# Kernel tuning notes

Hardware: AMD Instinct MI355X
Metric: run time of the kernel (lower is better)

The kernel has to match this reference:

```python
import jax, jax.numpy as jnp
import numpy as np
from jax import lax

BN_EPS = 1e-5


def _spatial_gate(x, w, g, b, m, v):
    # x: [N, C, H, W]; ChannelPool -> [N, 2, H, W]; 7x7 conv -> [N,1,H,W]; BN (eval); sigmoid gate
    comp = jnp.stack([jnp.max(x, axis=1), jnp.mean(x, axis=1)], axis=1)
    o = lax.conv_general_dilated(comp, w, (1, 1), [(3, 3), (3, 3)],
                                 dimension_numbers=('NCHW', 'OIHW', 'NCHW'))
    o = (o - m[None, :, None, None]) * lax.rsqrt(v + BN_EPS)[None, :, None, None] \
        * g[None, :, None, None] + b[None, :, None, None]
    s = jax.nn.sigmoid(o)
    return x * s


def _eca_sort(x, w_eca):
    # global avg pool -> sort channels desc -> 1D conv over sorted seq -> sigmoid -> unsort -> gate
    y = jnp.mean(x, axis=(2, 3))               # [N, C]
    order = jnp.argsort(-y, axis=1)            # descending sort indices
    rank = jnp.argsort(order, axis=1)          # inverse permutation
    ys = jnp.take_along_axis(y, order, axis=1)  # sorted descending
    k = w_eca.shape[-1]
    p = k // 2
    o = lax.conv_general_dilated(ys[:, None, :], w_eca, (1,), [(p, p)],
                                 dimension_numbers=('NCH', 'OIH', 'NCH'))[:, 0, :]
    sig = jax.nn.sigmoid(o)
    yr = jnp.take_along_axis(sig, rank, axis=1)  # reorder back per original index_select(rank)
    return x * yr[:, :, None, None]


def setup_inputs() -> dict:
    key = jax.random.key(0)
    ks = jax.random.split(key, 6)
    N, C, H, W = 32, 256, 56, 56
    inp = {
        'x': jax.random.normal(ks[0], (N, C, H, W), dtype=jnp.float32),
        'weight': jax.random.normal(ks[1], (1,), dtype=jnp.float32),
        'w_h': jax.random.normal(ks[2], (1, 2, 7, 7), dtype=jnp.float32) * 0.1,
        'g_h': jnp.ones((1,), jnp.float32), 'b_h': jnp.zeros((1,), jnp.float32),
        'm_h': jnp.zeros((1,), jnp.float32), 'v_h': jnp.ones((1,), jnp.float32),
        'w_w': jax.random.normal(ks[3], (1, 2, 7, 7), dtype=jnp.float32) * 0.1,
        'g_w': jnp.ones((1,), jnp.float32), 'b_w': jnp.zeros((1,), jnp.float32),
        'm_w': jnp.zeros((1,), jnp.float32), 'v_w': jnp.ones((1,), jnp.float32),
        'w_s': jax.random.normal(ks[4], (1, 2, 7, 7), dtype=jnp.float32) * 0.1,
        'g_s': jnp.ones((1,), jnp.float32), 'b_s': jnp.zeros((1,), jnp.float32),
        'm_s': jnp.zeros((1,), jnp.float32), 'v_s': jnp.ones((1,), jnp.float32),
        'w_eca': jax.random.normal(ks[5], (1, 1, 5), dtype=jnp.float32) * 0.3,
    }
    return inp


def reference(x, weight, w_h, g_h, b_h, m_h, v_h, w_w, g_w, b_w, m_w, v_w,
              w_s, g_s, b_s, m_s, v_s, w_eca):
    # branch 1: gate over H-as-channel (permute 0,2,1,3)
    xh = jnp.transpose(x, (0, 2, 1, 3))
    x11 = jnp.transpose(_spatial_gate(xh, w_h, g_h, b_h, m_h, v_h), (0, 2, 1, 3))
    # branch 2: gate over W-as-channel (permute 0,3,2,1)
    xw = jnp.transpose(x, (0, 3, 2, 1))
    x21 = jnp.transpose(_spatial_gate(xw, w_w, g_w, b_w, m_w, v_w), (0, 3, 2, 1))
    # branch 3: eca with sort/unsort
    x31 = _eca_sort(x, w_eca)
    # branch 4: plain spatial gate
    xo = _spatial_gate(x, w_s, g_s, b_s, m_s, v_s)
    return 0.23779 * xo + 0.24695 * x11 + 0.24365 * x21 + 0.27173 * x31
```

## Files before the change

### kernel.cpp

```cpp
#include <hip/hip_runtime.h>
#include <math.h>

#define N_ 32
#define C_ 256
#define H_ 56
#define W_ 56
#define HW_ (H_*W_)
#define HW4_ (HW_/4)
#define CHW_ (C_*HW_)
#define CHW4_ (CHW_/4)
#define NHW_ (N_*HW_)
#define NHW4_ (NHW_/4)
#define NCW_ (N_*C_*W_)
#define NHC_ (N_*H_*C_)
#define BN_EPS_ 1e-5f

#define TLD 57

#define F4MAX(a,b) do { (a).x=fmaxf((a).x,(b).x); (a).y=fmaxf((a).y,(b).y); \
                        (a).z=fmaxf((a).z,(b).z); (a).w=fmaxf((a).w,(b).w); } while(0)
#define F4ADD(a,b) do { (a).x+=(b).x; (a).y+=(b).y; (a).z+=(b).z; (a).w+=(b).w; } while(0)

__global__ __launch_bounds__(64) void plane_k(
        const float* __restrict__ x,
        float* __restrict__ maxH, float* __restrict__ meanH,
        float* __restrict__ maxWt, float* __restrict__ meanWt,
        float* __restrict__ y) {
    __shared__ float tile[H_ * TLD];
    const int wid = blockIdx.x;
    const int lane = threadIdx.x;
    const int n = wid >> 8, c = wid & 255;
    const float4* x4 = (const float4*)x + (size_t)wid * HW4_;

    float4 r[12], rl;
    #pragma unroll
    for (int i = 0; i < 12; ++i) r[i] = x4[i * 64 + lane];
    if (lane < 16) rl = x4[768 + lane];
    #pragma unroll
    for (int i = 0; i < 12; ++i) {
        int u = i * 64 + lane;
        int row = u / 14, c0 = (u - row * 14) * 4;
        float* d = &tile[row * TLD + c0];
        d[0] = r[i].x; d[1] = r[i].y; d[2] = r[i].z; d[3] = r[i].w;
    }
    if (lane < 16) {
        int u = 768 + lane;
        int row = u / 14, c0 = (u - row * 14) * 4;
        float* d = &tile[row * TLD + c0];
        d[0] = rl.x; d[1] = rl.y; d[2] = rl.z; d[3] = rl.w;
    }
    float csm = 0.f;
    if (lane < W_) {
        float cmx = -INFINITY;
        #pragma unroll 8
        for (int j = 0; j < H_; ++j) {
            float v = tile[j * TLD + lane];
            cmx = fmaxf(cmx, v); csm += v;
        }
        int o = (n * C_ + c) * W_ + lane;
        maxH[o] = cmx;
        meanH[o] = csm * (1.f / H_);
    }
    float ysum = (lane < W_) ? csm : 0.f;
    #pragma unroll
    for (int off = 32; off >= 1; off >>= 1) ysum += __shfl_xor(ysum, off);
    if (lane == 0) y[n * C_ + c] = ysum * (1.f / HW_);
    if (lane < H_) {
        const float* rp = &tile[lane * TLD];
        float rmx = -INFINITY, rsm = 0.f;
        #pragma unroll 8
        for (int j = 0; j < W_; ++j) {
            float v = rp[j];
            rmx = fmaxf(rmx, v); rsm += v;
        }
        int o = (n * C_ + c) * H_ + lane;
        maxWt[o] = rmx;
        meanWt[o] = rsm * (1.f / W_);
    }
}

__global__ __launch_bounds__(256) void cpool_k(
        const float* __restrict__ x,
        float* __restrict__ maxC, float* __restrict__ meanC) {
    __shared__ float4 smx[256];
    __shared__ float4 ssm[256];
    int bb = blockIdx.x;
    int tid = threadIdx.x;
    int g = tid >> 5, qi = tid & 31;
    int q = bb * 32 + qi;
    int n = q / HW4_;
    int hw4 = q - n * HW4_;
    const float4* x4 = (const float4*)x;
    size_t base = (size_t)n * CHW4_ + hw4 + (size_t)(g * 32) * HW4_;
    float4 mx = make_float4(-INFINITY, -INFINITY, -INFINITY, -INFINITY);
    float4 sm = make_float4(0.f, 0.f, 0.f, 0.f);
    #pragma unroll 16
    for (int i = 0; i < 32; ++i) {
        float4 v = x4[base + (size_t)i * HW4_];
        F4MAX(mx, v);
        F4ADD(sm, v);
    }
    smx[g * 32 + qi] = mx;
    ssm[g * 32 + qi] = sm;
    __syncthreads();
    if (tid < 32) {
        float4 m = smx[tid];
        #pragma unroll
        for (int j = 1; j < 8; ++j) F4MAX(m, smx[j * 32 + tid]);
        ((float4*)maxC)[bb * 32 + tid] = m;
    } else if (tid < 64) {
        int t2 = tid - 32;
        float4 s = ssm[t2];
        #pragma unroll
        for (int j = 1; j < 8; ++j) F4ADD(s, ssm[j * 32 + t2]);
        s.x *= (1.f / C_); s.y *= (1.f / C_); s.z *= (1.f / C_); s.w *= (1.f / C_);
        ((float4*)meanC)[bb * 32 + t2] = s;
    }
}

template <int R, int Cc, bool TR>
__device__ __forceinline__ void conv7_part(int t, const float* __restrict__ p0,
                                           const float* __restrict__ p1,
                                           const float* __restrict__ wt,
                                           float g, float bb, float m, float v,
                                           float* __restrict__ out) {
    const int per = R * Cc;
    int n = t / per;
    int r2 = t - n * per;
    int i = r2 / Cc, j = r2 - i * Cc;
    const float* b0 = p0 + (size_t)n * per;
    const float* b1 = p1 + (size_t)n * per;
    float acc = 0.f;
    #pragma unroll
    for (int ki = 0; ki < 7; ++ki) {
        int ii = i + ki - 3;
        if (ii < 0 || ii >= R) continue;
        #pragma unroll
        for (int kj = 0; kj < 7; ++kj) {
            int jj = j + kj - 3;
            if (jj < 0 || jj >= Cc) continue;
            int idx = ii * Cc + jj;
            int wi = TR ? (kj * 7 + ki) : (ki * 7 + kj);
            acc += b0[idx] * wt[wi] + b1[idx] * wt[49 + wi];
        }
    }
    float o = (acc - m) * rsqrtf(v + BN_EPS_) * g + bb;
    out[t] = 1.f / (1.f + expf(-o));
}

#define NB_SS (NHW_ / 256)
#define NB_SH (NCW_ / 256)
#define NB_SW (NHC_ / 256)

__global__ __launch_bounds__(256) void conv_eca_k(
        const float* __restrict__ maxC, const float* __restrict__ meanC,
        const float* __restrict__ maxH, const float* __restrict__ meanH,
        const float* __restrict__ maxWt, const float* __restrict__ meanWt,
        const float* __restrict__ w_s, const float* __restrict__ g_s,
        const float* __restrict__ b_s, const float* __restrict__ m_s,
        const float* __restrict__ v_s,
        const float* __restrict__ w_h, const float* __restrict__ g_h,
        const float* __restrict__ b_h, const float* __restrict__ m_h,
        const float* __restrict__ v_h,
        const float* __restrict__ w_w, const float* __restrict__ g_w,
        const float* __restrict__ b_w, const float* __restrict__ m_w,
        const float* __restrict__ v_w,
        const float* __restrict__ y, const float* __restrict__ w_eca,
        float* __restrict__ s_s, float* __restrict__ s_h, float* __restrict__ s_wt,
        float* __restrict__ gate) {
    __shared__ float sv[C_];
    __shared__ int si[C_];
    int b = blockIdx.x;
    int tid = threadIdx.x;
    if (b < NB_SS) {
        conv7_part<H_, W_, false>(b * 256 + tid, maxC, meanC, w_s, g_s[0], b_s[0],
                                  m_s[0], v_s[0], s_s);
    } else if (b < NB_SS + NB_SH) {
        conv7_part<C_, W_, false>((b - NB_SS) * 256 + tid, maxH, meanH, w_h, g_h[0],
                                  b_h[0], m_h[0], v_h[0], s_h);
    } else if (b < NB_SS + NB_SH + NB_SW) {
        conv7_part<C_, H_, true>((b - NB_SS - NB_SH) * 256 + tid, maxWt, meanWt, w_w,
                                 g_w[0], b_w[0], m_w[0], v_w[0], s_wt);
    } else {
        int n = b - (NB_SS + NB_SH + NB_SW);
        sv[tid] = y[n * C_ + tid];
        si[tid] = tid;
        __syncthreads();
        for (int k = 2; k <= C_; k <<= 1) {
            for (int j = k >> 1; j > 0; j >>= 1) {
                int ixj = tid ^ j;
                if (ixj > tid) {
                    float v1 = sv[tid], v2 = sv[ixj];
                    int i1 = si[tid], i2 = si[ixj];
                    bool before = (v1 > v2) || (v1 == v2 && i1 < i2);
                    bool dir = ((tid & k) == 0);
                    if (dir ? !before : before) {
                        sv[tid] = v2; sv[ixj] = v1;
                        si[tid] = i2; si[ixj] = i1;
                    }
                }
                __syncthreads();
            }
        }
        float o = 0.f;
        #pragma unroll
        for (int j = 0; j < 5; ++j) {
            int p = tid + j - 2;
            if (p >= 0 && p < C_) o += sv[p] * w_eca[j];
        }
        gate[n * C_ + si[tid]] = 1.f / (1.f + expf(-o));
    }
}

__global__ __launch_bounds__(256) void apply_k(
        const float* __restrict__ x, const float* __restrict__ s_s,
        const float* __restrict__ s_h, const float* __restrict__ s_wt,
        const float* __restrict__ gate, float* __restrict__ out) {
    int t0 = blockIdx.x * 512 + threadIdx.x;
    #pragma unroll
    for (int r = 0; r < 2; ++r) {
        int t = t0 + r * 256;
        int f = t * 4;
        int n = f / CHW_;
        int rem = f - n * CHW_;
        int c = rem / HW_;
        int hw = rem - c * HW_;
        int h = hw / W_;
        int w = hw - h * W_;
        float4 xv = ((const float4*)x)[t];
        float4 s4 = *(const float4*)(s_s + (size_t)n * HW_ + hw);
        float4 h4 = *(const float4*)(s_h + ((size_t)n * C_ + c) * W_ + w);
        float sw = s_wt[((size_t)n * C_ + c) * H_ + h];
        float ge = gate[n * C_ + c];
        float base = 0.24365f * sw + 0.27173f * ge;
        float4 o;
        o.x = xv.x * (0.23779f * s4.x + 0.24695f * h4.x + base);
        o.y = xv.y * (0.23779f * s4.y + 0.24695f * h4.y + base);
        o.z = xv.z * (0.23779f * s4.z + 0.24695f * h4.z + base);
        o.w = xv.w * (0.23779f * s4.w + 0.24695f * h4.w + base);
        ((float4*)out)[t] = o;
    }
}

extern "C" void kernel_launch(void* const* d_in, const int* in_sizes, int n_in,
                              void* d_out, int out_size, void* d_ws, size_t ws_size,
                              hipStream_t stream) {
    const float* x     = (const float*)d_in[0];
    const float* w_h   = (const float*)d_in[2];
    const float* g_h   = (const float*)d_in[3];
    const float* b_h   = (const float*)d_in[4];
    const float* m_h   = (const float*)d_in[5];
    const float* v_h   = (const float*)d_in[6];
    const float* w_w   = (const float*)d_in[7];
    const float* g_w   = (const float*)d_in[8];
    const float* b_w   = (const float*)d_in[9];
    const float* m_w   = (const float*)d_in[10];
    const float* v_w   = (const float*)d_in[11];
    const float* w_s   = (const float*)d_in[12];
    const float* g_s   = (const float*)d_in[13];
    const float* b_s   = (const float*)d_in[14];
    const float* m_s   = (const float*)d_in[15];
    const float* v_s   = (const float*)d_in[16];
    const float* w_eca = (const float*)d_in[17];
    float* out = (float*)d_out;

    float* ws    = (float*)d_ws;
    float* maxC  = ws;
    float* meanC = maxC  + NHW_;
    float* maxH  = meanC + NHW_;
    float* meanH = maxH  + NCW_;
    float* maxWt = meanH + NCW_;
    float* meanWt= maxWt + NHC_;
    float* s_s   = meanWt+ NHC_;
    float* s_h   = s_s   + NHW_;
    float* s_wt  = s_h   + NCW_;
    float* yv    = s_wt  + NHC_;
    float* gate  = yv    + N_ * C_;

    plane_k<<<N_ * C_, 64, 0, stream>>>(x, maxH, meanH, maxWt, meanWt, yv);

    cpool_k<<<NHW4_ / 32, 256, 0, stream>>>(x, maxC, meanC);

    int conv_blocks = NB_SS + NB_SH + NB_SW + N_;
    conv_eca_k<<<conv_blocks, 256, 0, stream>>>(maxC, meanC, maxH, meanH, maxWt, meanWt,
                                                w_s, g_s, b_s, m_s, v_s,
                                                w_h, g_h, b_h, m_h, v_h,
                                                w_w, g_w, b_w, m_w, v_w,
                                                yv, w_eca, s_s, s_h, s_wt, gate);

    apply_k<<<(N_ * CHW_ / 4) / 512, 256, 0, stream>>>(x, s_s, s_h, s_wt, gate, out);
}
```

Before: 100.5 us.

## Replace LDS-tiled plane reduction with wave-shuffle row/column reduction

The per-plane reduction kernel no longer stages the 56x56 plane in shared memory. Each wave now reads one row per iteration with scalar loads, keeps running column max and sum in registers, and reduces each row with a shuffle butterfly. Four planes are packed per 256-thread block. This removes LDS traffic and its occupancy limit, but loads become scalar instead of float4 and each row costs 12 shuffles, so the kernel does more ALU and cross-lane work.

After: 141.6 us. 40.9% more time.

```diff
diff --git a/kernel.cpp b/kernel.cpp
--- a/kernel.cpp
+++ b/kernel.cpp
@@ -15,68 +15,52 @@
 #define NHC_ (N_*H_*C_)
 #define BN_EPS_ 1e-5f
 
-#define TLD 57
-
 #define F4MAX(a,b) do { (a).x=fmaxf((a).x,(b).x); (a).y=fmaxf((a).y,(b).y); \
                         (a).z=fmaxf((a).z,(b).z); (a).w=fmaxf((a).w,(b).w); } while(0)
 #define F4ADD(a,b) do { (a).x+=(b).x; (a).y+=(b).y; (a).z+=(b).z; (a).w+=(b).w; } while(0)
 
-__global__ __launch_bounds__(64) void plane_k(
+__global__ __launch_bounds__(256) void rowcol_k(
         const float* __restrict__ x,
         float* __restrict__ maxH, float* __restrict__ meanH,
         float* __restrict__ maxWt, float* __restrict__ meanWt,
         float* __restrict__ y) {
-    __shared__ float tile[H_ * TLD];
-    const int wid = blockIdx.x;
-    const int lane = threadIdx.x;
+    const int wave = threadIdx.x >> 6;
+    const int lane = threadIdx.x & 63;
+    const int wid = blockIdx.x * 4 + wave;
     const int n = wid >> 8, c = wid & 255;
-    const float4* x4 = (const float4*)x + (size_t)wid * HW4_;
-
-    float4 r[12], rl;
-    #pragma unroll
-    for (int i = 0; i < 12; ++i) r[i] = x4[i * 64 + lane];
-    if (lane < 16) rl = x4[768 + lane];
-    #pragma unroll
-    for (int i = 0; i < 12; ++i) {
-        int u = i * 64 + lane;
-        int row = u / 14, c0 = (u - row * 14) * 4;
-        float* d = &tile[row * TLD + c0];
-        d[0] = r[i].x; d[1] = r[i].y; d[2] = r[i].z; d[3] = r[i].w;
-    }
-    if (lane < 16) {
-        int u = 768 + lane;
-        int row = u / 14, c0 = (u - row * 14) * 4;
-        float* d = &tile[row * TLD + c0];
-        d[0] = rl.x; d[1] = rl.y; d[2] = rl.z; d[3] = rl.w;
-    }
-    float csm = 0.f;
-    if (lane < W_) {
-        float cmx = -INFINITY;
-        #pragma unroll 8
-        for (int j = 0; j < H_; ++j) {
-            float v = tile[j * TLD + lane];
-            cmx = fmaxf(cmx, v); csm += v;
-        }
+    const float* p = x + (size_t)wid * HW_;
+    const bool act = lane < W_;
+    const int lc = act ? lane : (W_ - 1);
+
+    float cmx = -INFINITY, csm = 0.f;
+    float rmx_a = 0.f, rsm_a = 0.f;
+    float ysum = 0.f;
+
+    #pragma unroll 8
+    for (int h = 0; h < H_; ++h) {
+        float v = p[h * W_ + lc];
+        float vm = act ? v : -INFINITY;
+        float vs = act ? v : 0.f;
+        cmx = fmaxf(cmx, vm);
+        csm += vs;
+        float rm = vm, rs = vs;
+        #pragma unroll
+        for (int off = 32; off >= 1; off >>= 1) {
+            rm = fmaxf(rm, __shfl_xor(rm, off));
+            rs += __shfl_xor(rs, off);
+        }
+        if (lane == h) { rmx_a = rm; rsm_a = rs; }
+        ysum += rs;
+    }
+    if (act) {
         int o = (n * C_ + c) * W_ + lane;
         maxH[o] = cmx;
         meanH[o] = csm * (1.f / H_);
-    }
-    float ysum = (lane < W_) ? csm : 0.f;
-    #pragma unroll
-    for (int off = 32; off >= 1; off >>= 1) ysum += __shfl_xor(ysum, off);
+        int ot = (n * C_ + c) * H_ + lane;
+        maxWt[ot] = rmx_a;
+        meanWt[ot] = rsm_a * (1.f / W_);
+    }
     if (lane == 0) y[n * C_ + c] = ysum * (1.f / HW_);
-    if (lane < H_) {
-        const float* rp = &tile[lane * TLD];
-        float rmx = -INFINITY, rsm = 0.f;
-        #pragma unroll 8
-        for (int j = 0; j < W_; ++j) {
-            float v = rp[j];
-            rmx = fmaxf(rmx, v); rsm += v;
-        }
-        int o = (n * C_ + c) * H_ + lane;
-        maxWt[o] = rmx;
-        meanWt[o] = rsm * (1.f / W_);
-    }
 }
 
 __global__ __launch_bounds__(256) void cpool_k(
@@ -277,7 +261,7 @@
     float* yv    = s_wt  + NHC_;
     float* gate  = yv    + N_ * C_;
 
-    plane_k<<<N_ * C_, 64, 0, stream>>>(x, maxH, meanH, maxWt, meanWt, yv);
+    rowcol_k<<<(N_ * C_) / 4, 256, 0, stream>>>(x, maxH, meanH, maxWt, meanWt, yv);
 
     cpool_k<<<NHW4_ / 32, 256, 0, stream>>>(x, maxC, meanC);
 
```
